# Optimization experiments

Measured on AMD Instinct MI355X. Metric: run time of the kernel, lower is better.

Reference implementation:

```python
import jax, jax.numpy as jnp
import numpy as np

B, N, C, H = 2, 2048, 1024, 16
D = C // H  # head_dim = 64


def _rope_freqs(n, d_half, theta=10000.0):
    inv = 1.0 / (theta ** (np.arange(0, d_half, dtype=np.float32) / d_half))
    ang = np.arange(n, dtype=np.float32)[:, None] * inv[None, :]
    return jnp.asarray(np.cos(ang)), jnp.asarray(np.sin(ang))


def setup_inputs() -> dict:
    key = jax.random.key(0)
    ks = jax.random.split(key, 5)
    cos, sin = _rope_freqs(N, D // 2)
    s = 0.02
    return {
        "x": jax.random.normal(ks[0], (B, N, C), jnp.float32),
        "w_qkv": jax.random.normal(ks[1], (3 * C, C), jnp.float32) * s,
        "b_qkv": jnp.zeros((3 * C,), jnp.float32),
        "w_proj": jax.random.normal(ks[2], (C, C), jnp.float32) * s,
        "b_proj": jnp.zeros((C,), jnp.float32),
        "freqs_cos": cos,
        "freqs_sin": sin,
    }


def _apply_rope(t, cos, sin):
    # t: (B, H, N, D); consecutive pairs (even, odd) form complex numbers,
    # matching torch.view_as_complex on reshape(..., D//2, 2).
    te = t[..., 0::2]
    to = t[..., 1::2]
    cos = cos[None, None, :, :]  # (1,1,N,D//2)
    sin = sin[None, None, :, :]
    oe = te * cos - to * sin
    oo = te * sin + to * cos
    return jnp.stack([oe, oo], axis=-1).reshape(t.shape)


def reference(x, w_qkv, b_qkv, w_proj, b_proj, freqs_cos, freqs_sin):
    b, n, c = x.shape
    qkv = x @ w_qkv.T + b_qkv                      # (B,N,3C)
    qkv = qkv.reshape(b, n, 3, H, D).transpose(2, 0, 3, 1, 4)  # (3,B,H,N,D)
    q, k, v = qkv[0], qkv[1], qkv[2]
    q = _apply_rope(q, freqs_cos, freqs_sin)
    k = _apply_rope(k, freqs_cos, freqs_sin)
    scale = 1.0 / jnp.sqrt(jnp.asarray(D, x.dtype))
    scores = jnp.einsum("bhqd,bhkd->bhqk", q, k) * scale
    attn = jax.nn.softmax(scores, axis=-1)
    out = jnp.einsum("bhqk,bhkd->bhqd", attn, v)   # (B,H,N,D)
    out = out.transpose(0, 2, 1, 3).reshape(b, n, c)
    return out @ w_proj.T + b_proj
```

## Files before the change

### kernel.cpp

```cpp
#include <hip/hip_runtime.h>
#include <hip/hip_bf16.h>
#include <stdint.h>

#define BB 2
#define NN 2048
#define CC 1024
#define HH 16
#define DD 64
#define C3 3072

typedef __attribute__((ext_vector_type(8))) short bf16x8;
typedef __attribute__((ext_vector_type(4))) float f32x4;
typedef __attribute__((ext_vector_type(4))) unsigned short ushort4_t;

__device__ __forceinline__ unsigned short f2bf(float f) {
  union { float f; unsigned u; } v; v.f = f;
  unsigned r = v.u + 0x7FFFu + ((v.u >> 16) & 1u);
  return (unsigned short)(r >> 16);
}

#if __has_builtin(__builtin_amdgcn_exp2f)
#define EXP2(x) __builtin_amdgcn_exp2f(x)
#else
#define EXP2(x) exp2f(x)
#endif

#define QSCALE 0.18033688f

#define GLDS(g, l) __builtin_amdgcn_global_load_lds( \
    (const __attribute__((address_space(1))) void*)(g), \
    (__attribute__((address_space(3))) void*)(l), 16, 0, 0)

__global__ __launch_bounds__(256) void k_cvt(
    const float* __restrict__ x, const float* __restrict__ wq,
    const float* __restrict__ wp,
    unsigned short* __restrict__ xb, unsigned short* __restrict__ wqb,
    unsigned short* __restrict__ wpb)
{
  int blk = blockIdx.x;
  const float* s; unsigned short* d; int i;
  if (blk < 4096)      { s = x;  d = xb;  i = blk * 256 + threadIdx.x; }
  else if (blk < 7168) { s = wq; d = wqb; i = (blk - 4096) * 256 + threadIdx.x; }
  else                 { s = wp; d = wpb; i = (blk - 7168) * 256 + threadIdx.x; }
  float4 v = ((const float4*)s)[i];
  ushort4_t o;
  o.x = f2bf(v.x); o.y = f2bf(v.y); o.z = f2bf(v.z); o.w = f2bf(v.w);
  ((ushort4_t*)d)[i] = o;
}

__global__ __launch_bounds__(256) void k_gemm_qkv(
    const unsigned short* __restrict__ A, const unsigned short* __restrict__ Bt,
    const float* __restrict__ bias,
    const float* __restrict__ cosb, const float* __restrict__ sinb,
    unsigned short* __restrict__ Qg, unsigned short* __restrict__ Kg,
    unsigned short* __restrict__ Vt)
{
  __shared__ __align__(16) unsigned short Sh[16384];
  const int tid  = threadIdx.x;
  const int lane = tid & 63;
  const int wave = tid >> 6;
  const int bm = blockIdx.y * 128;
  const int bn = blockIdx.x * 128;
  const int wm = (wave >> 1) * 64;
  const int wn = (wave & 1) * 64;
  const int frow = lane & 15;
  const int fk   = (lane >> 4) * 8;
  const int K = 1024;
  const int NIT = K / 32;

  f32x4 acc[4][4] = {};

  const int row0 = tid >> 2, cc0 = tid & 3;
  const int row1 = row0 + 64;
  const unsigned short* Arow0 = A  + (size_t)(bm + row0) * K + cc0 * 8;
  const unsigned short* Arow1 = A  + (size_t)(bm + row1) * K + cc0 * 8;
  const unsigned short* Brow0 = Bt + (size_t)(bn + row0) * K + cc0 * 8;
  const unsigned short* Brow1 = Bt + (size_t)(bn + row1) * K + cc0 * 8;

  GLDS(Arow0, Sh + (size_t)tid * 8);
  GLDS(Brow0, Sh + 4096 + (size_t)tid * 8);
  GLDS(Arow1, Sh + (size_t)(tid + 256) * 8);
  GLDS(Brow1, Sh + 4096 + (size_t)(tid + 256) * 8);

  for (int it = 0; it < NIT; ++it) {
    const int p = it & 1;
    const unsigned short* As = Sh + p * 8192;
    const unsigned short* Bs = As + 4096;
    __syncthreads();

    if (it + 1 < NIT) {
      const int k1 = (it + 1) * 32;
      unsigned short* An = Sh + (1 - p) * 8192;
      GLDS(Arow0 + k1, An + (size_t)tid * 8);
      GLDS(Brow0 + k1, An + 4096 + (size_t)tid * 8);
      GLDS(Arow1 + k1, An + (size_t)(tid + 256) * 8);
      GLDS(Brow1 + k1, An + 4096 + (size_t)(tid + 256) * 8);
    }

    bf16x8 af[4], bfr[4];
#pragma unroll
    for (int t = 0; t < 4; ++t) {
      af[t]  = *(const bf16x8*)(As + (wm + t * 16 + frow) * 32 + fk);
      bfr[t] = *(const bf16x8*)(Bs + (wn + t * 16 + frow) * 32 + fk);
    }
#pragma unroll
    for (int mt = 0; mt < 4; ++mt)
#pragma unroll
      for (int nt = 0; nt < 4; ++nt)
        acc[mt][nt] = __builtin_amdgcn_mfma_f32_16x16x32_bf16(af[mt], bfr[nt], acc[mt][nt], 0, 0, 0);
  }
  __syncthreads();

  const int er0  = (lane >> 4) * 4;
  const int ecol = lane & 15;
  const int region = bn >> 10;
  const int gcol0 = bn + wn;
  const int h  = (gcol0 >> 6) & 15;
  const int rowg0 = bm + wm;
  const int b  = rowg0 >> 11;
  const int n0 = rowg0 & (NN - 1);
  unsigned short* wt = Sh + wave * 4096;

#pragma unroll
  for (int nt = 0; nt < 4; ++nt) {
    const int c64 = nt * 16 + ecol;
    const float bv = bias[gcol0 + c64];
    const int ii  = c64 >> 1;
#pragma unroll
    for (int mt = 0; mt < 4; ++mt)
#pragma unroll
      for (int r = 0; r < 4; ++r) {
        const int ml = mt * 16 + er0 + r;
        const int n  = n0 + ml;
        float v = acc[mt][nt][r] + bv;
        float vp = __shfl_xor(v, 1, 64);
        if (region == 2) {
          wt[c64 * 64 + ((((ml >> 3) ^ (c64 & 7)) << 3) | (ml & 7))] = f2bf(v);
        } else {
          float cth = cosb[n * 32 + ii], sth = sinb[n * 32 + ii];
          float ov = (c64 & 1) ? (vp * sth + v * cth)
                               : (v * cth - vp * sth);
          if (region == 0) ov *= QSCALE;
          wt[ml * 64 + ((((c64 >> 3) ^ (ml & 7)) << 3) | (c64 & 7))] = f2bf(ov);
        }
      }
  }

  const int rr = lane >> 3, cc = lane & 7;
  if (region == 2) {
    unsigned short* dst = Vt + (size_t)(b * HH + h) * DD * NN + n0;
#pragma unroll
    for (int it = 0; it < 8; ++it) {
      int dl = it * 8 + rr;
      bf16x8 vv = *(const bf16x8*)(wt + dl * 64 + ((cc ^ (dl & 7)) << 3));
      *(bf16x8*)(dst + (size_t)dl * NN + cc * 8) = vv;
    }
  } else {
    unsigned short* dqk = ((region == 0) ? Qg : Kg) +
                          ((size_t)(b * HH + h) * NN + n0) * DD;
#pragma unroll
    for (int it = 0; it < 8; ++it) {
      int ml = it * 8 + rr;
      bf16x8 vv = *(const bf16x8*)(wt + ml * 64 + ((cc ^ (ml & 7)) << 3));
      *(bf16x8*)(dqk + (size_t)ml * DD + cc * 8) = vv;
    }
  }
}

__global__ __launch_bounds__(256) void k_attn(
    const unsigned short* __restrict__ Qg, const unsigned short* __restrict__ Kg,
    const unsigned short* __restrict__ Vtg, unsigned short* __restrict__ Og)
{
  __shared__ __align__(16) unsigned short Ks[2][64 * 64];
  __shared__ __align__(16) unsigned short Vs[2][64 * 64];
  __shared__ __align__(16) unsigned short Ps[4][32 * 64];

  const int tid  = threadIdx.x;
  const int lane = tid & 63;
  const int wave = tid >> 6;
  const int bh = blockIdx.x >> 4;
  const int qt = blockIdx.x & 15;
  const int q0 = qt * 128 + wave * 32;
  const int frow   = lane & 15;
  const int fchunk = lane >> 4;
  const int er0  = (lane >> 4) * 4;
  const int ecol = lane & 15;

  const unsigned short* Qb = Qg  + (size_t)bh * NN * DD;
  const unsigned short* Kb = Kg  + (size_t)bh * NN * DD;
  const unsigned short* Vb = Vtg + (size_t)bh * DD * NN;

  bf16x8 qf[2][2];
#pragma unroll
  for (int m = 0; m < 2; ++m)
#pragma unroll
    for (int kt = 0; kt < 2; ++kt)
      qf[m][kt] = *(const bf16x8*)(Qb + (size_t)(q0 + m * 16 + frow) * DD + kt * 32 + fchunk * 8);

  bf16x8 ones;
#pragma unroll
  for (int i = 0; i < 8; ++i) ones[i] = (short)0x3F80;

  f32x4 oacc[2][4] = {};
  f32x4 lacc[2] = {};

  const int row0 = tid >> 3, cc0 = tid & 7;
  const int sw0 = (cc0 ^ (row0 & 7)) * 8;

  GLDS(Kb + (size_t)row0 * DD + sw0,        Ks[0] + (size_t)tid * 8);
  GLDS(Vb + (size_t)row0 * NN + sw0,        Vs[0] + (size_t)tid * 8);
  GLDS(Kb + (size_t)(row0 + 32) * DD + sw0, Ks[0] + (size_t)(tid + 256) * 8);
  GLDS(Vb + (size_t)(row0 + 32) * NN + sw0, Vs[0] + (size_t)(tid + 256) * 8);

  for (int t = 0; t < NN / 64; ++t) {
    const int p = t & 1;
    __syncthreads();

    if (t + 1 < NN / 64) {
      const int j = (t + 1) * 64;
      GLDS(Kb + (size_t)(j + row0) * DD + sw0,      Ks[1 - p] + (size_t)tid * 8);
      GLDS(Vb + (size_t)row0 * NN + j + sw0,        Vs[1 - p] + (size_t)tid * 8);
      GLDS(Kb + (size_t)(j + row0 + 32) * DD + sw0, Ks[1 - p] + (size_t)(tid + 256) * 8);
      GLDS(Vb + (size_t)(row0 + 32) * NN + j + sw0, Vs[1 - p] + (size_t)(tid + 256) * 8);
    }

    f32x4 sacc[2][4] = {};
#pragma unroll
    for (int nt = 0; nt < 4; ++nt) {
      int kr = nt * 16 + frow;
      bf16x8 kf0 = *(const bf16x8*)(Ks[p] + kr * 64 + ((fchunk       ^ (kr & 7)) << 3));
      bf16x8 kf1 = *(const bf16x8*)(Ks[p] + kr * 64 + (((fchunk + 4) ^ (kr & 7)) << 3));
#pragma unroll
      for (int m = 0; m < 2; ++m) {
        sacc[m][nt] = __builtin_amdgcn_mfma_f32_16x16x32_bf16(qf[m][0], kf0, sacc[m][nt], 0, 0, 0);
        sacc[m][nt] = __builtin_amdgcn_mfma_f32_16x16x32_bf16(qf[m][1], kf1, sacc[m][nt], 0, 0, 0);
      }
    }

#pragma unroll
    for (int m = 0; m < 2; ++m)
#pragma unroll
      for (int r = 0; r < 4; ++r) {
        int prow = m * 16 + er0 + r;
#pragma unroll
        for (int nt = 0; nt < 4; ++nt) {
          float pv = EXP2(sacc[m][nt][r]);
          union { float f; unsigned u; } cv; cv.f = pv;
          int col = nt * 16 + ecol;
          Ps[wave][prow * 64 + (((col >> 3) ^ (prow & 7)) << 3) + (col & 7)] =
              (unsigned short)(cv.u >> 16);
        }
      }

    bf16x8 pf0[2], pf1[2];
#pragma unroll
    for (int m = 0; m < 2; ++m) {
      int pr = m * 16 + frow;
      pf0[m] = *(const bf16x8*)(&Ps[wave][pr * 64 + ((fchunk       ^ (pr & 7)) << 3)]);
      pf1[m] = *(const bf16x8*)(&Ps[wave][pr * 64 + (((fchunk + 4) ^ (pr & 7)) << 3)]);
      lacc[m] = __builtin_amdgcn_mfma_f32_16x16x32_bf16(pf0[m], ones, lacc[m], 0, 0, 0);
      lacc[m] = __builtin_amdgcn_mfma_f32_16x16x32_bf16(pf1[m], ones, lacc[m], 0, 0, 0);
    }
#pragma unroll
    for (int dt = 0; dt < 4; ++dt) {
      int vr = dt * 16 + frow;
      bf16x8 vf0 = *(const bf16x8*)(Vs[p] + vr * 64 + ((fchunk       ^ (vr & 7)) << 3));
      bf16x8 vf1 = *(const bf16x8*)(Vs[p] + vr * 64 + (((fchunk + 4) ^ (vr & 7)) << 3));
#pragma unroll
      for (int m = 0; m < 2; ++m) {
        oacc[m][dt] = __builtin_amdgcn_mfma_f32_16x16x32_bf16(pf0[m], vf0, oacc[m][dt], 0, 0, 0);
        oacc[m][dt] = __builtin_amdgcn_mfma_f32_16x16x32_bf16(pf1[m], vf1, oacc[m][dt], 0, 0, 0);
      }
    }
  }

  const int b = bh >> 4;
  const int h = bh & 15;
#pragma unroll
  for (int m = 0; m < 2; ++m)
#pragma unroll
    for (int dt = 0; dt < 4; ++dt)
#pragma unroll
      for (int r = 0; r < 4; ++r) {
        int qrow = q0 + m * 16 + er0 + r;
        int d = dt * 16 + ecol;
        float v = oacc[m][dt][r] / lacc[m][r];
        Og[(size_t)(b * NN + qrow) * CC + h * DD + d] = f2bf(v);
      }
}

__global__ __launch_bounds__(256) void k_gemm_proj(
    const unsigned short* __restrict__ A, const unsigned short* __restrict__ Bt,
    const float* __restrict__ bias, float* __restrict__ Co)
{
  __shared__ __align__(16) unsigned short As[2][64 * 32];
  __shared__ __align__(16) unsigned short Bs[2][128 * 32];
  const int tid  = threadIdx.x;
  const int lane = tid & 63;
  const int wave = tid >> 6;
  const int bm = blockIdx.y * 64;
  const int bn = blockIdx.x * 128;
  const int wm = (wave >> 1) * 32;
  const int wn = (wave & 1) * 64;
  const int frow = lane & 15;
  const int fk   = (lane >> 4) * 8;
  const int K = 1024;
  const int NIT = K / 32;

  f32x4 acc[2][4] = {};

  const int row0 = tid >> 2, cc0 = tid & 3;
  const unsigned short* Arow  = A  + (size_t)(bm + row0) * K + cc0 * 8;
  const unsigned short* Brow0 = Bt + (size_t)(bn + row0) * K + cc0 * 8;
  const unsigned short* Brow1 = Bt + (size_t)(bn + row0 + 64) * K + cc0 * 8;

  GLDS(Arow,  As[0] + (size_t)tid * 8);
  GLDS(Brow0, Bs[0] + (size_t)tid * 8);
  GLDS(Brow1, Bs[0] + (size_t)(tid + 256) * 8);

  for (int it = 0; it < NIT; ++it) {
    const int p = it & 1;
    __syncthreads();

    if (it + 1 < NIT) {
      const int k1 = (it + 1) * 32;
      GLDS(Arow  + k1, As[1 - p] + (size_t)tid * 8);
      GLDS(Brow0 + k1, Bs[1 - p] + (size_t)tid * 8);
      GLDS(Brow1 + k1, Bs[1 - p] + (size_t)(tid + 256) * 8);
    }

    bf16x8 af[2], bfr[4];
#pragma unroll
    for (int t = 0; t < 2; ++t)
      af[t] = *(const bf16x8*)(As[p] + (wm + t * 16 + frow) * 32 + fk);
#pragma unroll
    for (int t = 0; t < 4; ++t)
      bfr[t] = *(const bf16x8*)(Bs[p] + (wn + t * 16 + frow) * 32 + fk);
#pragma unroll
    for (int mt = 0; mt < 2; ++mt)
#pragma unroll
      for (int nt = 0; nt < 4; ++nt)
        acc[mt][nt] = __builtin_amdgcn_mfma_f32_16x16x32_bf16(af[mt], bfr[nt], acc[mt][nt], 0, 0, 0);
  }

  const int er0  = (lane >> 4) * 4;
  const int ecol = lane & 15;
#pragma unroll
  for (int nt = 0; nt < 4; ++nt) {
    int col = bn + wn + nt * 16 + ecol;
    float bv = bias[col];
#pragma unroll
    for (int mt = 0; mt < 2; ++mt)
#pragma unroll
      for (int r = 0; r < 4; ++r) {
        int rowg = bm + wm + mt * 16 + er0 + r;
        Co[(size_t)rowg * CC + col] = acc[mt][nt][r] + bv;
      }
  }
}

extern "C" void kernel_launch(void* const* d_in, const int* in_sizes, int n_in,
                              void* d_out, int out_size, void* d_ws, size_t ws_size,
                              hipStream_t stream)
{
  const float* x      = (const float*)d_in[0];
  const float* w_qkv  = (const float*)d_in[1];
  const float* b_qkv  = (const float*)d_in[2];
  const float* w_proj = (const float*)d_in[3];
  const float* b_proj = (const float*)d_in[4];
  const float* fcos   = (const float*)d_in[5];
  const float* fsin   = (const float*)d_in[6];
  float* out = (float*)d_out;

  char* ws = (char*)d_ws;
  unsigned short* xb     = (unsigned short*)(ws);
  unsigned short* wqkvb  = (unsigned short*)(ws + 8388608);
  unsigned short* wprojb = (unsigned short*)(ws + 14680064);
  unsigned short* Qb     = (unsigned short*)(ws + 16777216);
  unsigned short* Kb     = (unsigned short*)(ws + 25165824);
  unsigned short* Vtb    = (unsigned short*)(ws + 33554432);
  unsigned short* aob    = (unsigned short*)(ws + 41943040);

  k_cvt<<<8192, 256, 0, stream>>>(x, w_qkv, w_proj, xb, wqkvb, wprojb);

  k_gemm_qkv<<<dim3(24, 32), 256, 0, stream>>>(xb, wqkvb, b_qkv, fcos, fsin,
                                               Qb, Kb, Vtb);

  k_attn<<<512, 256, 0, stream>>>(Qb, Kb, Vtb, aob);

  k_gemm_proj<<<dim3(8, 64), 256, 0, stream>>>(aob, wprojb, b_proj, out);
}
```

Measured before the change: 226.6 us.

## Keep softmax probabilities in registers via transposed S and 16x16x16 MFMA

```diff
diff --git a/kernel.cpp b/kernel.cpp
--- a/kernel.cpp
+++ b/kernel.cpp
@@ -10,6 +10,7 @@
 #define C3 3072
 
 typedef __attribute__((ext_vector_type(8))) short bf16x8;
+typedef __attribute__((ext_vector_type(4))) short bf16x4;
 typedef __attribute__((ext_vector_type(4))) float f32x4;
 typedef __attribute__((ext_vector_type(4))) unsigned short ushort4_t;
 
@@ -24,6 +25,19 @@
 #else
 #define EXP2(x) exp2f(x)
 #endif
+
+#if __has_builtin(__builtin_amdgcn_mfma_f32_16x16x16bf16_1k)
+#define HAVE_MFMA16 1
+#endif
+
+__device__ __forceinline__ unsigned pack_bf2(float a, float b) {
+  union { float f; unsigned u; } ua, ub; ua.f = a; ub.f = b;
+#if __has_builtin(__builtin_amdgcn_perm)
+  return __builtin_amdgcn_perm(ub.u, ua.u, 0x07060302u);
+#else
+  return (ua.u >> 16) | (ub.u & 0xFFFF0000u);
+#endif
+}
 
 #define QSCALE 0.18033688f
 
@@ -173,7 +187,9 @@
 {
   __shared__ __align__(16) unsigned short Ks[2][64 * 64];
   __shared__ __align__(16) unsigned short Vs[2][64 * 64];
+#ifndef HAVE_MFMA16
   __shared__ __align__(16) unsigned short Ps[4][32 * 64];
+#endif
 
   const int tid  = threadIdx.x;
   const int lane = tid & 63;
@@ -197,12 +213,7 @@
     for (int kt = 0; kt < 2; ++kt)
       qf[m][kt] = *(const bf16x8*)(Qb + (size_t)(q0 + m * 16 + frow) * DD + kt * 32 + fchunk * 8);
 
-  bf16x8 ones;
-#pragma unroll
-  for (int i = 0; i < 8; ++i) ones[i] = (short)0x3F80;
-
   f32x4 oacc[2][4] = {};
-  f32x4 lacc[2] = {};
 
   const int row0 = tid >> 3, cc0 = tid & 7;
   const int sw0 = (cc0 ^ (row0 & 7)) * 8;
@@ -211,6 +222,9 @@
   GLDS(Vb + (size_t)row0 * NN + sw0,        Vs[0] + (size_t)tid * 8);
   GLDS(Kb + (size_t)(row0 + 32) * DD + sw0, Ks[0] + (size_t)(tid + 256) * 8);
   GLDS(Vb + (size_t)(row0 + 32) * NN + sw0, Vs[0] + (size_t)(tid + 256) * 8);
+
+#ifdef HAVE_MFMA16
+  float lsum[2] = {0.f, 0.f};
 
   for (int t = 0; t < NN / 64; ++t) {
     const int p = t & 1;
@@ -232,11 +246,91 @@
       bf16x8 kf1 = *(const bf16x8*)(Ks[p] + kr * 64 + (((fchunk + 4) ^ (kr & 7)) << 3));
 #pragma unroll
       for (int m = 0; m < 2; ++m) {
+        sacc[m][nt] = __builtin_amdgcn_mfma_f32_16x16x32_bf16(kf0, qf[m][0], sacc[m][nt], 0, 0, 0);
+        sacc[m][nt] = __builtin_amdgcn_mfma_f32_16x16x32_bf16(kf1, qf[m][1], sacc[m][nt], 0, 0, 0);
+      }
+    }
+
+    bf16x4 pfr[2][4];
+#pragma unroll
+    for (int m = 0; m < 2; ++m)
+#pragma unroll
+      for (int nt = 0; nt < 4; ++nt) {
+        float e0 = EXP2(sacc[m][nt][0]);
+        float e1 = EXP2(sacc[m][nt][1]);
+        float e2 = EXP2(sacc[m][nt][2]);
+        float e3 = EXP2(sacc[m][nt][3]);
+        lsum[m] += (e0 + e1) + (e2 + e3);
+        union { unsigned u[2]; bf16x4 v; } pk;
+        pk.u[0] = pack_bf2(e0, e1);
+        pk.u[1] = pack_bf2(e2, e3);
+        pfr[m][nt] = pk.v;
+      }
+
+#pragma unroll
+    for (int dt = 0; dt < 4; ++dt) {
+      int vr = dt * 16 + frow;
+      bf16x4 vfr[4];
+#pragma unroll
+      for (int c = 0; c < 4; ++c)
+        vfr[c] = *(const bf16x4*)(Vs[p] + vr * 64 +
+                   (((2 * c + (fchunk >> 1)) ^ (vr & 7)) << 3) + (fchunk & 1) * 4);
+#pragma unroll
+      for (int m = 0; m < 2; ++m)
+#pragma unroll
+        for (int c = 0; c < 4; ++c)
+          oacc[m][dt] = __builtin_amdgcn_mfma_f32_16x16x16bf16_1k(pfr[m][c], vfr[c], oacc[m][dt], 0, 0, 0);
+    }
+  }
+
+  const int b = bh >> 4;
+  const int h = bh & 15;
+#pragma unroll
+  for (int m = 0; m < 2; ++m) {
+    lsum[m] += __shfl_xor(lsum[m], 16, 64);
+    lsum[m] += __shfl_xor(lsum[m], 32, 64);
+    float linv[4];
+#pragma unroll
+    for (int r = 0; r < 4; ++r)
+      linv[r] = 1.0f / __shfl(lsum[m], er0 + r, 64);
+#pragma unroll
+    for (int dt = 0; dt < 4; ++dt)
+#pragma unroll
+      for (int r = 0; r < 4; ++r) {
+        int qrow = q0 + m * 16 + er0 + r;
+        int d = dt * 16 + ecol;
+        Og[(size_t)(b * NN + qrow) * CC + h * DD + d] = f2bf(oacc[m][dt][r] * linv[r]);
+      }
+  }
+
+#else
+  bf16x8 ones;
+#pragma unroll
+  for (int i = 0; i < 8; ++i) ones[i] = (short)0x3F80;
+  f32x4 lacc[2] = {};
+
+  for (int t = 0; t < NN / 64; ++t) {
+    const int p = t & 1;
+    __syncthreads();
+    if (t + 1 < NN / 64) {
+      const int j = (t + 1) * 64;
+      GLDS(Kb + (size_t)(j + row0) * DD + sw0,      Ks[1 - p] + (size_t)tid * 8);
+      GLDS(Vb + (size_t)row0 * NN + j + sw0,        Vs[1 - p] + (size_t)tid * 8);
+      GLDS(Kb + (size_t)(j + row0 + 32) * DD + sw0, Ks[1 - p] + (size_t)(tid + 256) * 8);
+      GLDS(Vb + (size_t)(row0 + 32) * NN + j + sw0, Vs[1 - p] + (size_t)(tid + 256) * 8);
+    }
+    f32x4 sacc[2][4] = {};
+#pragma unroll
+    for (int nt = 0; nt < 4; ++nt) {
+      int kr = nt * 16 + frow;
+      bf16x8 kf0 = *(const bf16x8*)(Ks[p] + kr * 64 + ((fchunk       ^ (kr & 7)) << 3));
+      bf16x8 kf1 = *(const bf16x8*)(Ks[p] + kr * 64 + (((fchunk + 4) ^ (kr & 7)) << 3));
+#pragma unroll
+      for (int m = 0; m < 2; ++m) {
         sacc[m][nt] = __builtin_amdgcn_mfma_f32_16x16x32_bf16(qf[m][0], kf0, sacc[m][nt], 0, 0, 0);
         sacc[m][nt] = __builtin_amdgcn_mfma_f32_16x16x32_bf16(qf[m][1], kf1, sacc[m][nt], 0, 0, 0);
       }
     }
-
 #pragma unroll
     for (int m = 0; m < 2; ++m)
 #pragma unroll
@@ -251,7 +345,6 @@
               (unsigned short)(cv.u >> 16);
         }
       }
-
     bf16x8 pf0[2], pf1[2];
 #pragma unroll
     for (int m = 0; m < 2; ++m) {
@@ -273,7 +366,6 @@
       }
     }
   }
-
   const int b = bh >> 4;
   const int h = bh & 15;
 #pragma unroll
@@ -284,9 +376,9 @@
       for (int r = 0; r < 4; ++r) {
         int qrow = q0 + m * 16 + er0 + r;
         int d = dt * 16 + ecol;
-        float v = oacc[m][dt][r] / lacc[m][r];
-        Og[(size_t)(b * NN + qrow) * CC + h * DD + d] = f2bf(v);
-      }
+        Og[(size_t)(b * NN + qrow) * CC + h * DD + d] = f2bf(oacc[m][dt][r] / lacc[m][r]);
+      }
+#endif
 }
 
 __global__ __launch_bounds__(256) void k_gemm_proj(
```

Result: faster. 212.5 us (-6.3%).

## Keep softmax probabilities in registers, widen KV tiles, narrow QKV GEMM tiles

Applied to the files above, without the earlier changes.

```diff
diff --git a/kernel.cpp b/kernel.cpp
--- a/kernel.cpp
+++ b/kernel.cpp
@@ -10,6 +10,7 @@
 #define C3 3072
 
 typedef __attribute__((ext_vector_type(8))) short bf16x8;
+typedef __attribute__((ext_vector_type(4))) short bf16x4;
 typedef __attribute__((ext_vector_type(4))) float f32x4;
 typedef __attribute__((ext_vector_type(4))) unsigned short ushort4_t;
 
@@ -24,6 +25,15 @@
 #else
 #define EXP2(x) exp2f(x)
 #endif
+
+__device__ __forceinline__ unsigned pack_bf2(float a, float b) {
+  union { float f; unsigned u; } ua, ub; ua.f = a; ub.f = b;
+#if __has_builtin(__builtin_amdgcn_perm)
+  return __builtin_amdgcn_perm(ub.u, ua.u, 0x07060302u);
+#else
+  return (ua.u >> 16) | (ub.u & 0xFFFF0000u);
+#endif
+}
 
 #define QSCALE 0.18033688f
 
@@ -55,58 +65,55 @@
     unsigned short* __restrict__ Qg, unsigned short* __restrict__ Kg,
     unsigned short* __restrict__ Vt)
 {
-  __shared__ __align__(16) unsigned short Sh[16384];
+  __shared__ __align__(16) unsigned short Sh[12288];
   const int tid  = threadIdx.x;
   const int lane = tid & 63;
   const int wave = tid >> 6;
   const int bm = blockIdx.y * 128;
-  const int bn = blockIdx.x * 128;
+  const int bn = blockIdx.x * 64;
   const int wm = (wave >> 1) * 64;
-  const int wn = (wave & 1) * 64;
+  const int wn = (wave & 1) * 32;
   const int frow = lane & 15;
   const int fk   = (lane >> 4) * 8;
   const int K = 1024;
   const int NIT = K / 32;
 
-  f32x4 acc[4][4] = {};
-
-  const int row0 = tid >> 2, cc0 = tid & 3;
-  const int row1 = row0 + 64;
-  const unsigned short* Arow0 = A  + (size_t)(bm + row0) * K + cc0 * 8;
-  const unsigned short* Arow1 = A  + (size_t)(bm + row1) * K + cc0 * 8;
-  const unsigned short* Brow0 = Bt + (size_t)(bn + row0) * K + cc0 * 8;
-  const unsigned short* Brow1 = Bt + (size_t)(bn + row1) * K + cc0 * 8;
+  f32x4 acc[4][2] = {};
+
+  const int arow0 = tid >> 2, cc0 = tid & 3;
+  const unsigned short* Arow0 = A  + (size_t)(bm + arow0) * K + cc0 * 8;
+  const unsigned short* Arow1 = A  + (size_t)(bm + arow0 + 64) * K + cc0 * 8;
+  const unsigned short* Brow  = Bt + (size_t)(bn + arow0) * K + cc0 * 8;
 
   GLDS(Arow0, Sh + (size_t)tid * 8);
-  GLDS(Brow0, Sh + 4096 + (size_t)tid * 8);
   GLDS(Arow1, Sh + (size_t)(tid + 256) * 8);
-  GLDS(Brow1, Sh + 4096 + (size_t)(tid + 256) * 8);
+  GLDS(Brow,  Sh + 4096 + (size_t)tid * 8);
 
   for (int it = 0; it < NIT; ++it) {
     const int p = it & 1;
-    const unsigned short* As = Sh + p * 8192;
+    const unsigned short* As = Sh + p * 6144;
     const unsigned short* Bs = As + 4096;
     __syncthreads();
 
     if (it + 1 < NIT) {
       const int k1 = (it + 1) * 32;
-      unsigned short* An = Sh + (1 - p) * 8192;
+      unsigned short* An = Sh + (1 - p) * 6144;
       GLDS(Arow0 + k1, An + (size_t)tid * 8);
-      GLDS(Brow0 + k1, An + 4096 + (size_t)tid * 8);
       GLDS(Arow1 + k1, An + (size_t)(tid + 256) * 8);
-      GLDS(Brow1 + k1, An + 4096 + (size_t)(tid + 256) * 8);
-    }
-
-    bf16x8 af[4], bfr[4];
-#pragma unroll
-    for (int t = 0; t < 4; ++t) {
+      GLDS(Brow  + k1, An + 4096 + (size_t)tid * 8);
+    }
+
+    bf16x8 af[4], bfr[2];
+#pragma unroll
+    for (int t = 0; t < 4; ++t)
       af[t]  = *(const bf16x8*)(As + (wm + t * 16 + frow) * 32 + fk);
+#pragma unroll
+    for (int t = 0; t < 2; ++t)
       bfr[t] = *(const bf16x8*)(Bs + (wn + t * 16 + frow) * 32 + fk);
-    }
 #pragma unroll
     for (int mt = 0; mt < 4; ++mt)
 #pragma unroll
-      for (int nt = 0; nt < 4; ++nt)
+      for (int nt = 0; nt < 2; ++nt)
         acc[mt][nt] = __builtin_amdgcn_mfma_f32_16x16x32_bf16(af[mt], bfr[nt], acc[mt][nt], 0, 0, 0);
   }
   __syncthreads();
@@ -115,16 +122,18 @@
   const int ecol = lane & 15;
   const int region = bn >> 10;
   const int gcol0 = bn + wn;
-  const int h  = (gcol0 >> 6) & 15;
+  const int h     = (gcol0 >> 6) & 15;
+  const int dbase = gcol0 & 63;
   const int rowg0 = bm + wm;
   const int b  = rowg0 >> 11;
   const int n0 = rowg0 & (NN - 1);
-  unsigned short* wt = Sh + wave * 4096;
-
-#pragma unroll
-  for (int nt = 0; nt < 4; ++nt) {
-    const int c64 = nt * 16 + ecol;
-    const float bv = bias[gcol0 + c64];
+  unsigned short* wt = Sh + wave * 2048;
+
+#pragma unroll
+  for (int nt = 0; nt < 2; ++nt) {
+    const int cloc = nt * 16 + ecol;
+    const int c64  = dbase + cloc;
+    const float bv = bias[gcol0 + nt * 16 + ecol];
     const int ii  = c64 >> 1;
 #pragma unroll
     for (int mt = 0; mt < 4; ++mt)
@@ -135,33 +144,34 @@
         float v = acc[mt][nt][r] + bv;
         float vp = __shfl_xor(v, 1, 64);
         if (region == 2) {
-          wt[c64 * 64 + ((((ml >> 3) ^ (c64 & 7)) << 3) | (ml & 7))] = f2bf(v);
+          wt[cloc * 64 + ((((ml >> 3) ^ (cloc & 7)) << 3) | (ml & 7))] = f2bf(v);
         } else {
           float cth = cosb[n * 32 + ii], sth = sinb[n * 32 + ii];
           float ov = (c64 & 1) ? (vp * sth + v * cth)
                                : (v * cth - vp * sth);
           if (region == 0) ov *= QSCALE;
-          wt[ml * 64 + ((((c64 >> 3) ^ (ml & 7)) << 3) | (c64 & 7))] = f2bf(ov);
+          wt[ml * 32 + ((((cloc >> 3) ^ (ml & 3)) << 3) | (cloc & 7))] = f2bf(ov);
         }
       }
   }
 
-  const int rr = lane >> 3, cc = lane & 7;
   if (region == 2) {
-    unsigned short* dst = Vt + (size_t)(b * HH + h) * DD * NN + n0;
-#pragma unroll
-    for (int it = 0; it < 8; ++it) {
+    const int rr = lane >> 3, cc = lane & 7;
+    unsigned short* dst = Vt + ((size_t)(b * HH + h) * DD + dbase) * NN + n0;
+#pragma unroll
+    for (int it = 0; it < 4; ++it) {
       int dl = it * 8 + rr;
       bf16x8 vv = *(const bf16x8*)(wt + dl * 64 + ((cc ^ (dl & 7)) << 3));
       *(bf16x8*)(dst + (size_t)dl * NN + cc * 8) = vv;
     }
   } else {
+    const int rr = lane >> 2, cc = lane & 3;
     unsigned short* dqk = ((region == 0) ? Qg : Kg) +
-                          ((size_t)(b * HH + h) * NN + n0) * DD;
-#pragma unroll
-    for (int it = 0; it < 8; ++it) {
-      int ml = it * 8 + rr;
-      bf16x8 vv = *(const bf16x8*)(wt + ml * 64 + ((cc ^ (ml & 7)) << 3));
+                          ((size_t)(b * HH + h) * NN + n0) * DD + dbase;
+#pragma unroll
+    for (int it = 0; it < 4; ++it) {
+      int ml = it * 16 + rr;
+      bf16x8 vv = *(const bf16x8*)(wt + ml * 32 + ((cc ^ (ml & 3)) << 3));
       *(bf16x8*)(dqk + (size_t)ml * DD + cc * 8) = vv;
     }
   }
@@ -171,9 +181,8 @@
     const unsigned short* __restrict__ Qg, const unsigned short* __restrict__ Kg,
     const unsigned short* __restrict__ Vtg, unsigned short* __restrict__ Og)
 {
-  __shared__ __align__(16) unsigned short Ks[2][64 * 64];
-  __shared__ __align__(16) unsigned short Vs[2][64 * 64];
-  __shared__ __align__(16) unsigned short Ps[4][32 * 64];
+  __shared__ __align__(16) unsigned short Ks[2][128 * 64];
+  __shared__ __align__(16) unsigned short Vs[2][64 * 128];
 
   const int tid  = threadIdx.x;
   const int lane = tid & 63;
@@ -197,79 +206,78 @@
     for (int kt = 0; kt < 2; ++kt)
       qf[m][kt] = *(const bf16x8*)(Qb + (size_t)(q0 + m * 16 + frow) * DD + kt * 32 + fchunk * 8);
 
-  bf16x8 ones;
-#pragma unroll
-  for (int i = 0; i < 8; ++i) ones[i] = (short)0x3F80;
-
   f32x4 oacc[2][4] = {};
-  f32x4 lacc[2] = {};
-
-  const int row0 = tid >> 3, cc0 = tid & 7;
-  const int sw0 = (cc0 ^ (row0 & 7)) * 8;
-
-  GLDS(Kb + (size_t)row0 * DD + sw0,        Ks[0] + (size_t)tid * 8);
-  GLDS(Vb + (size_t)row0 * NN + sw0,        Vs[0] + (size_t)tid * 8);
-  GLDS(Kb + (size_t)(row0 + 32) * DD + sw0, Ks[0] + (size_t)(tid + 256) * 8);
-  GLDS(Vb + (size_t)(row0 + 32) * NN + sw0, Vs[0] + (size_t)(tid + 256) * 8);
-
-  for (int t = 0; t < NN / 64; ++t) {
+  float lsum[2] = {0.f, 0.f};
+
+  const int krow0 = tid >> 3;
+  const int ksw = ((tid & 7) ^ (krow0 & 7)) * 8;
+  const int vrow0 = tid >> 4, vc = tid & 15;
+  const int vsw = (((vc ^ (vrow0 & 7)) & 7) | (vc & 8)) * 8;
+
+#pragma unroll
+  for (int k = 0; k < 4; ++k) {
+    GLDS(Kb + (size_t)(krow0 + 32 * k) * DD + ksw, Ks[0] + (size_t)(tid + 256 * k) * 8);
+    GLDS(Vb + (size_t)(vrow0 + 16 * k) * NN + vsw, Vs[0] + (size_t)(tid + 256 * k) * 8);
+  }
+
+  for (int t = 0; t < NN / 128; ++t) {
     const int p = t & 1;
     __syncthreads();
 
-    if (t + 1 < NN / 64) {
-      const int j = (t + 1) * 64;
-      GLDS(Kb + (size_t)(j + row0) * DD + sw0,      Ks[1 - p] + (size_t)tid * 8);
-      GLDS(Vb + (size_t)row0 * NN + j + sw0,        Vs[1 - p] + (size_t)tid * 8);
-      GLDS(Kb + (size_t)(j + row0 + 32) * DD + sw0, Ks[1 - p] + (size_t)(tid + 256) * 8);
-      GLDS(Vb + (size_t)(row0 + 32) * NN + j + sw0, Vs[1 - p] + (size_t)(tid + 256) * 8);
-    }
-
-    f32x4 sacc[2][4] = {};
-#pragma unroll
-    for (int nt = 0; nt < 4; ++nt) {
-      int kr = nt * 16 + frow;
-      bf16x8 kf0 = *(const bf16x8*)(Ks[p] + kr * 64 + ((fchunk       ^ (kr & 7)) << 3));
-      bf16x8 kf1 = *(const bf16x8*)(Ks[p] + kr * 64 + (((fchunk + 4) ^ (kr & 7)) << 3));
-#pragma unroll
-      for (int m = 0; m < 2; ++m) {
-        sacc[m][nt] = __builtin_amdgcn_mfma_f32_16x16x32_bf16(qf[m][0], kf0, sacc[m][nt], 0, 0, 0);
-        sacc[m][nt] = __builtin_amdgcn_mfma_f32_16x16x32_bf16(qf[m][1], kf1, sacc[m][nt], 0, 0, 0);
-      }
-    }
-
-#pragma unroll
-    for (int m = 0; m < 2; ++m)
-#pragma unroll
-      for (int r = 0; r < 4; ++r) {
-        int prow = m * 16 + er0 + r;
+    if (t + 1 < NN / 128) {
+      const int j = (t + 1) * 128;
+#pragma unroll
+      for (int k = 0; k < 4; ++k) {
+        GLDS(Kb + (size_t)(j + krow0 + 32 * k) * DD + ksw, Ks[1 - p] + (size_t)(tid + 256 * k) * 8);
+        GLDS(Vb + (size_t)(vrow0 + 16 * k) * NN + j + vsw, Vs[1 - p] + (size_t)(tid + 256 * k) * 8);
+      }
+    }
+
+#pragma unroll
+    for (int sub = 0; sub < 2; ++sub) {
+      f32x4 sacc[2][4] = {};
+#pragma unroll
+      for (int nt = 0; nt < 4; ++nt) {
+        int kr = sub * 64 + nt * 16 + frow;
+        bf16x8 kf0 = *(const bf16x8*)(Ks[p] + kr * 64 + ((fchunk       ^ (kr & 7)) << 3));
+        bf16x8 kf1 = *(const bf16x8*)(Ks[p] + kr * 64 + (((fchunk + 4) ^ (kr & 7)) << 3));
+#pragma unroll
+        for (int m = 0; m < 2; ++m) {
+          sacc[m][nt] = __builtin_amdgcn_mfma_f32_16x16x32_bf16(kf0, qf[m][0], sacc[m][nt], 0, 0, 0);
+          sacc[m][nt] = __builtin_amdgcn_mfma_f32_16x16x32_bf16(kf1, qf[m][1], sacc[m][nt], 0, 0, 0);
+        }
+      }
+
+      bf16x4 pfr[2][4];
+#pragma unroll
+      for (int m = 0; m < 2; ++m)
 #pragma unroll
         for (int nt = 0; nt < 4; ++nt) {
-          float pv = EXP2(sacc[m][nt][r]);
-          union { float f; unsigned u; } cv; cv.f = pv;
-          int col = nt * 16 + ecol;
-          Ps[wave][prow * 64 + (((col >> 3) ^ (prow & 7)) << 3) + (col & 7)] =
-              (unsigned short)(cv.u >> 16);
+          float e0 = EXP2(sacc[m][nt][0]);
+          float e1 = EXP2(sacc[m][nt][1]);
+          float e2 = EXP2(sacc[m][nt][2]);
+          float e3 = EXP2(sacc[m][nt][3]);
+          lsum[m] += (e0 + e1) + (e2 + e3);
+          union { unsigned u[2]; bf16x4 v; } pk;
+          pk.u[0] = pack_bf2(e0, e1);
+          pk.u[1] = pack_bf2(e2, e3);
+          pfr[m][nt] = pk.v;
         }
-      }
-
-    bf16x8 pf0[2], pf1[2];
-#pragma unroll
-    for (int m = 0; m < 2; ++m) {
-      int pr = m * 16 + frow;
-      pf0[m] = *(const bf16x8*)(&Ps[wave][pr * 64 + ((fchunk       ^ (pr & 7)) << 3)]);
-      pf1[m] = *(const bf16x8*)(&Ps[wave][pr * 64 + (((fchunk + 4) ^ (pr & 7)) << 3)]);
-      lacc[m] = __builtin_amdgcn_mfma_f32_16x16x32_bf16(pf0[m], ones, lacc[m], 0, 0, 0);
-      lacc[m] = __builtin_amdgcn_mfma_f32_16x16x32_bf16(pf1[m], ones, lacc[m], 0, 0, 0);
-    }
-#pragma unroll
-    for (int dt = 0; dt < 4; ++dt) {
-      int vr = dt * 16 + frow;
-      bf16x8 vf0 = *(const bf16x8*)(Vs[p] + vr * 64 + ((fchunk       ^ (vr & 7)) << 3));
-      bf16x8 vf1 = *(const bf16x8*)(Vs[p] + vr * 64 + (((fchunk + 4) ^ (vr & 7)) << 3));
-#pragma unroll
-      for (int m = 0; m < 2; ++m) {
-        oacc[m][dt] = __builtin_amdgcn_mfma_f32_16x16x32_bf16(pf0[m], vf0, oacc[m][dt], 0, 0, 0);
-        oacc[m][dt] = __builtin_amdgcn_mfma_f32_16x16x32_bf16(pf1[m], vf1, oacc[m][dt], 0, 0, 0);
+
+#pragma unroll
+      for (int dt = 0; dt < 4; ++dt) {
+        int vr = dt * 16 + frow;
+        bf16x4 vfr[4];
+#pragma unroll
+        for (int c = 0; c < 4; ++c) {
+          int l3 = ((2 * c + (fchunk >> 1)) ^ (vr & 7)) & 7;
+          vfr[c] = *(const bf16x4*)(Vs[p] + vr * 128 + ((sub * 8 + l3) << 3) + (fchunk & 1) * 4);
+        }
+#pragma unroll
+        for (int m = 0; m < 2; ++m)
+#pragma unroll
+          for (int c = 0; c < 4; ++c)
+            oacc[m][dt] = __builtin_amdgcn_mfma_f32_16x16x16bf16_1k(pfr[m][c], vfr[c], oacc[m][dt], 0, 0, 0);
       }
     }
   }
@@ -277,16 +285,22 @@
   const int b = bh >> 4;
   const int h = bh & 15;
 #pragma unroll
-  for (int m = 0; m < 2; ++m)
+  for (int m = 0; m < 2; ++m) {
+    lsum[m] += __shfl_xor(lsum[m], 16, 64);
+    lsum[m] += __shfl_xor(lsum[m], 32, 64);
+    float linv[4];
+#pragma unroll
+    for (int r = 0; r < 4; ++r)
+      linv[r] = 1.0f / __shfl(lsum[m], er0 + r, 64);
 #pragma unroll
     for (int dt = 0; dt < 4; ++dt)
 #pragma unroll
       for (int r = 0; r < 4; ++r) {
         int qrow = q0 + m * 16 + er0 + r;
         int d = dt * 16 + ecol;
-        float v = oacc[m][dt][r] / lacc[m][r];
-        Og[(size_t)(b * NN + qrow) * CC + h * DD + d] = f2bf(v);
-      }
+        Og[(size_t)(b * NN + qrow) * CC + h * DD + d] = f2bf(oacc[m][dt][r] * linv[r]);
+      }
+  }
 }
 
 __global__ __launch_bounds__(256) void k_gemm_proj(
@@ -383,7 +397,7 @@
 
   k_cvt<<<8192, 256, 0, stream>>>(x, w_qkv, w_proj, xb, wqkvb, wprojb);
 
-  k_gemm_qkv<<<dim3(24, 32), 256, 0, stream>>>(xb, wqkvb, b_qkv, fcos, fsin,
+  k_gemm_qkv<<<dim3(48, 32), 256, 0, stream>>>(xb, wqkvb, b_qkv, fcos, fsin,
                                                Qb, Kb, Vtb);
 
   k_attn<<<512, 256, 0, stream>>>(Qb, Kb, Vtb, aob);
```

Result: faster. 222.2 us (-2.0%).
